# Kernel tuning notes

Measured on AMD Instinct MI355X. Metric: run time of the kernel, lower is better.

## Reference

```python
import jax, jax.numpy as jnp
import numpy as np

N, E, IN, H, C, ED = 50000, 400000, 128, 16, 32, 16
NEG_SLOPE = 0.2

def setup_inputs() -> dict:
    key = jax.random.key(0)
    ks = jax.random.split(key, 9)
    x = jax.random.normal(ks[0], (N, IN), jnp.float32)
    edge_index = jax.random.randint(ks[1], (2, E), 0, N, dtype=jnp.int32)
    edge_attr = jax.random.normal(ks[2], (E, ED), jnp.float32)
    batch = jnp.zeros((N,), jnp.int32)
    W_l = jax.random.normal(ks[3], (IN, H * C), jnp.float32) * 0.05
    W_r = jax.random.normal(ks[4], (IN, H * C), jnp.float32) * 0.05
    att = jax.random.normal(ks[5], (H, C), jnp.float32) * 0.05
    bias_gat = jax.random.normal(ks[6], (C,), jnp.float32) * 0.05
    W_res = jax.random.normal(ks[7], (IN, C), jnp.float32) * 0.05
    return {"x": x, "edge_index": edge_index, "edge_attr": edge_attr, "batch": batch,
            "W_l": W_l, "W_r": W_r, "att": att, "bias_gat": bias_gat, "W_res": W_res}

def reference(x, edge_index, edge_attr, batch, W_l, W_r, att, bias_gat, W_res):
    # GATv2Conv (heads=16, concat=False, add_self_loops=True, edge_dim=None so
    # edge_attr is unused; dropout is inference no-op), then ReLU + projected residual.
    n = x.shape[0]
    loops = jnp.arange(n, dtype=edge_index.dtype)
    src = jnp.concatenate([edge_index[0], loops])  # message source j
    dst = jnp.concatenate([edge_index[1], loops])  # message target i
    xl = (x @ W_l).reshape(n, H, C)  # source transform
    xr = (x @ W_r).reshape(n, H, C)  # target transform
    # GATv2 score: e_ij = a^T LeakyReLU(xl_j + xr_i), per head. [Etot, H]
    e = jnp.einsum('ehc,hc->eh', jax.nn.leaky_relu(xl[src] + xr[dst], NEG_SLOPE), att)
    # segment softmax over incoming edges of each destination node
    m = jax.lax.stop_gradient(jax.ops.segment_max(e, dst, num_segments=n))
    ex = jnp.exp(e - m[dst])
    s = jax.ops.segment_sum(ex, dst, num_segments=n)
    alpha = ex / (s[dst] + 1e-16)  # [Etot, H]
    # weighted scatter-aggregate of source messages
    out = jax.ops.segment_sum(xl[src] * alpha[:, :, None], dst, num_segments=n)  # [N, H, C]
    gat_out = out.mean(axis=1) + bias_gat  # concat=False -> head mean, + bias
    x_out = jax.nn.relu(gat_out) + x @ W_res  # ReLU then SkipConnection projection
    return (x_out, alpha)
```

## Files before the change

kernel.cpp:

```cpp
#include <hip/hip_runtime.h>
#include <hip/hip_bf16.h>

typedef unsigned int u32;
typedef unsigned short u16;

typedef __attribute__((ext_vector_type(8))) short bf16x8;
typedef __attribute__((ext_vector_type(4))) float f32x4;

__device__ __forceinline__ float bflo(u32 p){ union{u32 u; float f;} v; v.u = p << 16; return v.f; }
__device__ __forceinline__ float bfhi(u32 p){ union{u32 u; float f;} v; v.u = p & 0xFFFF0000u; return v.f; }
__device__ __forceinline__ u16 f2bf(float f){
    union{float f; u32 u;} v; v.f = f;
    u32 r = (v.u + 0x7FFFu + ((v.u >> 16) & 1u)) >> 16;
    return (u16)r;
}
__device__ __forceinline__ u32 pack2(float a, float b){
    return ((u32)f2bf(a)) | (((u32)f2bf(b)) << 16);
}

#define HH 16
#define CC 32
#define HC 512
#define KIN 128
#define CT 1056
#define RESCALE_THR 8.0f

__global__ __launch_bounds__(256) void k_xconv(
    const float* __restrict__ x, u16* __restrict__ xb, int total)
{
    int t = blockIdx.x * 256 + threadIdx.x;
    if (t * 8 >= total) return;
    const float4* src = (const float4*)(x + (size_t)t * 8);
    float4 a = src[0], b = src[1];
    uint4 o;
    o.x = pack2(a.x, a.y); o.y = pack2(a.z, a.w);
    o.z = pack2(b.x, b.y); o.w = pack2(b.z, b.w);
    ((uint4*)xb)[t] = o;
}

__global__ __launch_bounds__(128) void k_wconv(
    const float* __restrict__ Wl, const float* __restrict__ Wr,
    const float* __restrict__ Wres, u16* __restrict__ wbt_frag)
{
    int c = blockIdx.x;
    int t = threadIdx.x;
    int k = t;
    float v;
    if (c < 512)       v = Wl[(size_t)k * 512 + c];
    else if (c < 1024) v = Wr[(size_t)k * 512 + (c - 512)];
    else               v = Wres[(size_t)k * 32 + (c - 1024)];
    int e    = k & 7;
    int krow = k >> 3;
    int kk   = krow >> 2;
    int lane = ((krow & 3) << 4) | (c & 15);
    int ct   = c >> 4;
    wbt_frag[(((size_t)ct * 4 + kk) * 64 + lane) * 8 + e] = f2bf(v);
}

__global__ __launch_bounds__(256) void k_mfma(
    const u16* __restrict__ xb, const u16* __restrict__ wbt_frag,
    u16* __restrict__ xl, u16* __restrict__ xr, float* __restrict__ xres,
    int N, int nrb)
{
    __shared__ u16 sh[128 * 128];
    const int i = blockIdx.x;
    const int xcd = i & 7;
    const int j = i >> 3;
    const int rb = xcd + 8 * (j / 9);
    const int cb = j % 9;
    if (rb >= nrb) return;
    const int tid = threadIdx.x;
    const int wave = tid >> 6, lane = tid & 63;
    const int row0 = rb * 128;

    uint4 zero = {0, 0, 0, 0};
    #pragma unroll
    for (int it = 0; it < 8; it++) {
        int idx = tid + it * 256;
        int r = idx >> 4, ch = idx & 15;
        int grow = row0 + r;
        uint4 v = (grow < N) ? ((const uint4*)(xb + (size_t)grow * KIN))[ch] : zero;
        *(uint4*)(sh + r * 128 + ((ch ^ (r & 7)) * 8)) = v;
    }
    __syncthreads();

    bf16x8 afrag[2][4];
    #pragma unroll
    for (int mt = 0; mt < 2; mt++) {
        #pragma unroll
        for (int kk = 0; kk < 4; kk++) {
            int r = wave * 32 + mt * 16 + (lane & 15);
            int chunk = (kk * 4 + (lane >> 4)) ^ (r & 7);
            afrag[mt][kk] = *(const bf16x8*)(sh + r * 128 + chunk * 8);
        }
    }
    __syncthreads();

    if (cb < 8) {
        #pragma unroll
        for (int nt = 0; nt < 8; nt++) {
            int ct = cb * 8 + nt;
            const bf16x8* bp = (const bf16x8*)(wbt_frag + (((size_t)ct * 4) * 64 + lane) * 8);
            f32x4 acc0 = {0, 0, 0, 0}, acc1 = {0, 0, 0, 0};
            #pragma unroll
            for (int kk = 0; kk < 4; kk++) {
                bf16x8 bfrag = bp[kk * 64];
                acc0 = __builtin_amdgcn_mfma_f32_16x16x32_bf16(afrag[0][kk], bfrag, acc0, 0, 0, 0);
                acc1 = __builtin_amdgcn_mfma_f32_16x16x32_bf16(afrag[1][kk], bfrag, acc1, 0, 0, 0);
            }
            int lcol = nt * 16 + (lane & 15);
            int ch = lcol >> 3, cin = lcol & 7;
            #pragma unroll
            for (int mt = 0; mt < 2; mt++) {
                f32x4 a = (mt == 0) ? acc0 : acc1;
                int rbase = wave * 32 + mt * 16 + (lane >> 4) * 4;
                #pragma unroll
                for (int jj = 0; jj < 4; jj++) {
                    int row = rbase + jj;
                    int chs = ch ^ ((row >> 2) & 3);
                    sh[row * 128 + chs * 8 + cin] = f2bf(a[jj]);
                }
            }
        }
        __syncthreads();
        u16* out = (cb < 4) ? xl : xr;
        const int colbase = (cb & 3) * 128;
        #pragma unroll
        for (int it = 0; it < 8; it++) {
            int idx = tid + it * 256;
            int r = idx >> 4, ch = idx & 15;
            int grow = row0 + r;
            if (grow < N) {
                int chs = ch ^ ((r >> 2) & 3);
                uint4 v = *(const uint4*)(sh + r * 128 + chs * 8);
                *(uint4*)(out + (size_t)grow * HC + colbase + ch * 8) = v;
            }
        }
    } else {
        #pragma unroll
        for (int nt = 0; nt < 2; nt++) {
            int ct = 64 + nt;
            const bf16x8* bp = (const bf16x8*)(wbt_frag + (((size_t)ct * 4) * 64 + lane) * 8);
            f32x4 acc0 = {0, 0, 0, 0}, acc1 = {0, 0, 0, 0};
            #pragma unroll
            for (int kk = 0; kk < 4; kk++) {
                bf16x8 bfrag = bp[kk * 64];
                acc0 = __builtin_amdgcn_mfma_f32_16x16x32_bf16(afrag[0][kk], bfrag, acc0, 0, 0, 0);
                acc1 = __builtin_amdgcn_mfma_f32_16x16x32_bf16(afrag[1][kk], bfrag, acc1, 0, 0, 0);
            }
            int c_out = nt * 16 + (lane & 15);
            #pragma unroll
            for (int mt = 0; mt < 2; mt++) {
                f32x4 a = (mt == 0) ? acc0 : acc1;
                int rbse = row0 + wave * 32 + mt * 16 + (lane >> 4) * 4;
                #pragma unroll
                for (int jj = 0; jj < 4; jj++) {
                    int grow = rbse + jj;
                    if (grow < N) xres[(size_t)grow * CC + c_out] = a[jj];
                }
            }
        }
    }
}

__global__ __launch_bounds__(256) void k_count(
    const int* __restrict__ ei, int* __restrict__ counts, int E, int N)
{
    int e = blockIdx.x * 256 + threadIdx.x;
    if (e >= E + N) return;
    int dst = (e < E) ? ei[E + e] : e - E;
    atomicAdd(&counts[dst], 1);
}

__global__ __launch_bounds__(1024) void k_scan1(
    const int* __restrict__ counts, int* __restrict__ offs, int* __restrict__ partials, int N)
{
    __shared__ int sh[1024];
    int i = blockIdx.x * 1024 + threadIdx.x;
    int v = (i < N) ? counts[i] : 0;
    sh[threadIdx.x] = v;
    __syncthreads();
    for (int off = 1; off < 1024; off <<= 1) {
        int t = (threadIdx.x >= off) ? sh[threadIdx.x - off] : 0;
        __syncthreads();
        sh[threadIdx.x] += t;
        __syncthreads();
    }
    if (i < N) offs[i] = sh[threadIdx.x] - v;
    if (threadIdx.x == 1023) partials[blockIdx.x] = sh[1023];
}

__global__ void k_scan2(int* __restrict__ partials, int nb)
{
    if (threadIdx.x == 0 && blockIdx.x == 0) {
        int run = 0;
        for (int k = 0; k < nb; k++) { int t = partials[k]; partials[k] = run; run += t; }
    }
}

__global__ __launch_bounds__(1024) void k_scan3(
    int* __restrict__ offs, const int* __restrict__ partials, int* __restrict__ cursor, int N)
{
    int i = blockIdx.x * 1024 + threadIdx.x;
    if (i < N) {
        int o = offs[i] + partials[blockIdx.x];
        offs[i] = o;
        cursor[i] = o;
    }
}

__global__ __launch_bounds__(256) void k_scatter(
    const int* __restrict__ ei, int* __restrict__ cursor,
    int* __restrict__ src_sorted, int* __restrict__ eid_sorted, int E, int N)
{
    int e = blockIdx.x * 256 + threadIdx.x;
    if (e >= E + N) return;
    int src, dst;
    if (e < E) { src = ei[e]; dst = ei[E + e]; }
    else       { src = e - E; dst = src; }
    int pos = atomicAdd(&cursor[dst], 1);
    src_sorted[pos] = src;
    eid_sorted[pos] = e;
}

__global__ __launch_bounds__(256) void k_fused(
    const int* __restrict__ src_sorted, const int* __restrict__ eid_sorted,
    const int* __restrict__ offs, const int* __restrict__ counts,
    const u16* __restrict__ xl, const u16* __restrict__ xr, const float* __restrict__ att,
    float* __restrict__ e_out, float2* __restrict__ ms_buf,
    float* __restrict__ out_mean, int N)
{
    int wid = (blockIdx.x * 256 + threadIdx.x) >> 6;
    int lane = threadIdx.x & 63;
    if (wid >= N) return;
    const int node = wid;

    uint4 b = ((const uint4*)(xr + (size_t)node * HC))[lane];
    float xrv[8] = { bflo(b.x), bfhi(b.x), bflo(b.y), bfhi(b.y),
                     bflo(b.z), bfhi(b.z), bflo(b.w), bfhi(b.w) };
    float4 w0 = ((const float4*)att)[lane * 2];
    float4 w1 = ((const float4*)att)[lane * 2 + 1];
    float wv[8] = { w0.x, w0.y, w0.z, w0.w, w1.x, w1.y, w1.z, w1.w };

    float m = -3.402823466e38f, s = 0.f;
    float acc[8] = {0, 0, 0, 0, 0, 0, 0, 0};

    const int beg = offs[node];
    const int deg = counts[node];
    const int h = lane >> 2;

    for (int base = 0; base < deg; base += 64) {
        int cnt = min(64, deg - base);
        int my_src = 0, my_eid = 0;
        if (lane < cnt) {
            my_src = src_sorted[beg + base + lane];
            my_eid = eid_sorted[beg + base + lane];
        }
        int s0 = __shfl(my_src, 0);
        uint4 a = ((const uint4*)(xl + (size_t)s0 * HC))[lane];
        for (int t = 0; t < cnt; t++) {
            uint4 ac = a;
            {
                int sn = __shfl(my_src, min(t + 1, cnt - 1));
                a = ((const uint4*)(xl + (size_t)sn * HC))[lane];
            }
            float xv[8] = { bflo(ac.x), bfhi(ac.x), bflo(ac.y), bfhi(ac.y),
                            bflo(ac.z), bfhi(ac.z), bflo(ac.w), bfhi(ac.w) };
            float esum = 0.f;
            #pragma unroll
            for (int q = 0; q < 8; q++) {
                float v = xv[q] + xrv[q];
                v = fmaxf(v, 0.2f * v);
                esum = fmaf(v, wv[q], esum);
            }
            esum += __shfl_xor(esum, 1);
            esum += __shfl_xor(esum, 2);

            int eid = __shfl(my_eid, t);
            if ((lane & 3) == 0)
                e_out[(size_t)eid * HH + h] = esum;

            if (__any(esum > m + RESCALE_THR)) {
                float mn = fmaxf(m, esum);
                float sc = __expf(m - mn);
                float p  = __expf(esum - mn);
                s = s * sc + p;
                m = mn;
                #pragma unroll
                for (int q = 0; q < 8; q++) acc[q] = fmaf(p, xv[q], acc[q] * sc);
            } else {
                float p = __expf(esum - m);
                s += p;
                #pragma unroll
                for (int q = 0; q < 8; q++) acc[q] = fmaf(p, xv[q], acc[q]);
            }
        }
    }

    float inv = 1.f / (s + 1e-16f);
    if ((lane & 3) == 0)
        ms_buf[(size_t)node * HH + h] = make_float2(m, inv);

    #pragma unroll
    for (int q = 0; q < 8; q++) acc[q] *= inv;
    #pragma unroll
    for (int st = 4; st <= 32; st <<= 1) {
        #pragma unroll
        for (int q = 0; q < 8; q++) acc[q] += __shfl_xor(acc[q], st);
    }
    if (lane < 4) {
        float* dp = out_mean + (size_t)node * CC + lane * 8;
        #pragma unroll
        for (int q = 0; q < 8; q++) dp[q] = acc[q];
    }
}

__global__ __launch_bounds__(256) void k_alpha(
    const int* __restrict__ ei, float* __restrict__ alpha,
    const float2* __restrict__ ms_buf, int E, int N)
{
    long long i = (long long)blockIdx.x * 256 + threadIdx.x;
    long long tot = (long long)(E + N) * HH;
    if (i >= tot) return;
    int edge = (int)(i >> 4);
    int h = (int)(i & 15);
    int dst = (edge < E) ? ei[E + edge] : edge - E;
    float2 ms = ms_buf[(size_t)dst * HH + h];
    alpha[i] = __expf(alpha[i] - ms.x) * ms.y;
}

__global__ __launch_bounds__(256) void k_final(
    const float* __restrict__ out_mean, const float* __restrict__ xres,
    const float* __restrict__ bias, float* __restrict__ x_out, int N)
{
    int i = blockIdx.x * 256 + threadIdx.x;
    if (i >= N * CC) return;
    int c = i & 31;
    float g = out_mean[i] * (1.f / 16.f) + bias[c];
    g = g > 0.f ? g : 0.f;
    x_out[i] = g + xres[i];
}

extern "C" void kernel_launch(void* const* d_in, const int* in_sizes, int n_in,
                              void* d_out, int out_size, void* d_ws, size_t ws_size,
                              hipStream_t stream)
{
    const int N = in_sizes[0] / KIN;
    const int E = in_sizes[1] / 2;
    const int Etot = E + N;

    const float* x    = (const float*)d_in[0];
    const int*   ei   = (const int*)d_in[1];
    const float* Wl   = (const float*)d_in[4];
    const float* Wr   = (const float*)d_in[5];
    const float* att  = (const float*)d_in[6];
    const float* bias = (const float*)d_in[7];
    const float* Wres = (const float*)d_in[8];

    char* ws = (char*)d_ws;
    u16*   xl         = (u16*)ws;   ws += (size_t)N * HC * 2;
    u16*   xr         = (u16*)ws;   ws += (size_t)N * HC * 2;
    float2* ms_buf    = (float2*)ws; ws += (size_t)N * HH * 8;
    float* xres       = (float*)ws; ws += (size_t)N * CC * 4;
    float* out_mean   = (float*)ws; ws += (size_t)N * CC * 4;
    int*   counts     = (int*)ws;   ws += (size_t)N * 4;
    int*   offs       = (int*)ws;   ws += (size_t)N * 4;
    int*   cursor     = (int*)ws;   ws += (size_t)N * 4;
    int*   partials   = (int*)ws;   ws += 256;
    int*   src_sorted = (int*)ws;   ws += (size_t)Etot * 4;
    int*   eid_sorted = (int*)ws;   ws += (size_t)Etot * 4;
    u16*   xb         = (u16*)ws;   ws += (size_t)N * KIN * 2;
    u16*   wbt_frag   = (u16*)ws;   ws += (size_t)CT * KIN * 2;

    float* x_out     = (float*)d_out;
    float* alpha_out = x_out + (size_t)N * CC;

    hipMemsetAsync(counts, 0, (size_t)N * 4, stream);

    int xtot = N * KIN;
    k_xconv<<<(xtot / 8 + 255) / 256, 256, 0, stream>>>(x, xb, xtot);
    k_wconv<<<CT, 128, 0, stream>>>(Wl, Wr, Wres, wbt_frag);

    int nrb = (N + 127) / 128;
    int mgrid = 8 * ((nrb + 7) / 8) * 9;
    k_mfma<<<mgrid, 256, 0, stream>>>(xb, wbt_frag, xl, xr, xres, N, nrb);

    int eg = (Etot + 255) / 256;
    k_count<<<eg, 256, 0, stream>>>(ei, counts, E, N);

    int nb = (N + 1023) / 1024;
    k_scan1<<<nb, 1024, 0, stream>>>(counts, offs, partials, N);
    k_scan2<<<1, 64, 0, stream>>>(partials, nb);
    k_scan3<<<nb, 1024, 0, stream>>>(offs, partials, cursor, N);

    k_scatter<<<eg, 256, 0, stream>>>(ei, cursor, src_sorted, eid_sorted, E, N);

    k_fused<<<(N * 64 + 255) / 256, 256, 0, stream>>>(
        src_sorted, eid_sorted, offs, counts, xl, xr, att,
        alpha_out, ms_buf, out_mean, N);

    int ag = (int)(((long long)Etot * HH + 255) / 256);
    k_alpha<<<ag, 256, 0, stream>>>(ei, alpha_out, ms_buf, E, N);

    k_final<<<(N * CC + 255) / 256, 256, 0, stream>>>(out_mean, xres, bias, x_out, N);
}
```

Baseline: 213.6 us.

## Fuse prep, scan and epilogue kernels; packed f32x2 math in aggregation

Merges the x/weight conversion and the counts memset into one prep kernel. It replaces the serial scan2 plus scan3 pair with a single kernel that reduces the partials per block, and merges the alpha-normalise and final-output kernels. This removes several launches and the single-thread scan pass. The aggregation kernel now runs one 64-thread block per node, reads src and eid indices directly instead of staging them through shuffles, and uses packed 2-wide float ops meant to map to packed FP32 instructions. Per-edge scalar index loads and the smaller blocks may add load latency and scheduling overhead.

```diff
diff --git a/kernel.cpp b/kernel.cpp
--- a/kernel.cpp
+++ b/kernel.cpp
@@ -6,6 +6,7 @@
 
 typedef __attribute__((ext_vector_type(8))) short bf16x8;
 typedef __attribute__((ext_vector_type(4))) float f32x4;
+typedef __attribute__((ext_vector_type(2))) float f32x2;
 
 __device__ __forceinline__ float bflo(u32 p){ union{u32 u; float f;} v; v.u = p << 16; return v.f; }
 __device__ __forceinline__ float bfhi(u32 p){ union{u32 u; float f;} v; v.u = p & 0xFFFF0000u; return v.f; }
@@ -25,36 +26,37 @@
 #define CT 1056
 #define RESCALE_THR 8.0f
 
-__global__ __launch_bounds__(256) void k_xconv(
-    const float* __restrict__ x, u16* __restrict__ xb, int total)
+__global__ __launch_bounds__(256) void k_prep(
+    const float* __restrict__ x, const float* __restrict__ Wl,
+    const float* __restrict__ Wr, const float* __restrict__ Wres,
+    u16* __restrict__ xb, u16* __restrict__ wbt_frag, int* __restrict__ counts,
+    int xq, int N)
 {
     int t = blockIdx.x * 256 + threadIdx.x;
-    if (t * 8 >= total) return;
-    const float4* src = (const float4*)(x + (size_t)t * 8);
-    float4 a = src[0], b = src[1];
-    uint4 o;
-    o.x = pack2(a.x, a.y); o.y = pack2(a.z, a.w);
-    o.z = pack2(b.x, b.y); o.w = pack2(b.z, b.w);
-    ((uint4*)xb)[t] = o;
-}
-
-__global__ __launch_bounds__(128) void k_wconv(
-    const float* __restrict__ Wl, const float* __restrict__ Wr,
-    const float* __restrict__ Wres, u16* __restrict__ wbt_frag)
-{
-    int c = blockIdx.x;
-    int t = threadIdx.x;
-    int k = t;
-    float v;
-    if (c < 512)       v = Wl[(size_t)k * 512 + c];
-    else if (c < 1024) v = Wr[(size_t)k * 512 + (c - 512)];
-    else               v = Wres[(size_t)k * 32 + (c - 1024)];
-    int e    = k & 7;
-    int krow = k >> 3;
-    int kk   = krow >> 2;
-    int lane = ((krow & 3) << 4) | (c & 15);
-    int ct   = c >> 4;
-    wbt_frag[(((size_t)ct * 4 + kk) * 64 + lane) * 8 + e] = f2bf(v);
+    if (t < xq) {
+        const float4* src = (const float4*)(x + (size_t)t * 8);
+        float4 a = src[0], b = src[1];
+        uint4 o;
+        o.x = pack2(a.x, a.y); o.y = pack2(a.z, a.w);
+        o.z = pack2(b.x, b.y); o.w = pack2(b.z, b.w);
+        ((uint4*)xb)[t] = o;
+    } else if (t < xq + CT * 128) {
+        int u = t - xq;
+        int c = u >> 7;
+        int k = u & 127;
+        float v;
+        if (c < 512)       v = Wl[(size_t)k * 512 + c];
+        else if (c < 1024) v = Wr[(size_t)k * 512 + (c - 512)];
+        else               v = Wres[(size_t)k * 32 + (c - 1024)];
+        int e    = k & 7;
+        int krow = k >> 3;
+        int kk   = krow >> 2;
+        int lane = ((krow & 3) << 4) | (c & 15);
+        int ct   = c >> 4;
+        wbt_frag[(((size_t)ct * 4 + kk) * 64 + lane) * 8 + e] = f2bf(v);
+    } else if (t < xq + CT * 128 + N) {
+        counts[t - xq - CT * 128] = 0;
+    }
 }
 
 __global__ __launch_bounds__(256) void k_mfma(
@@ -190,20 +192,22 @@
     if (threadIdx.x == 1023) partials[blockIdx.x] = sh[1023];
 }
 
-__global__ void k_scan2(int* __restrict__ partials, int nb)
-{
-    if (threadIdx.x == 0 && blockIdx.x == 0) {
-        int run = 0;
-        for (int k = 0; k < nb; k++) { int t = partials[k]; partials[k] = run; run += t; }
-    }
-}
-
-__global__ __launch_bounds__(1024) void k_scan3(
-    int* __restrict__ offs, const int* __restrict__ partials, int* __restrict__ cursor, int N)
-{
+__global__ __launch_bounds__(1024) void k_scan3f(
+    int* __restrict__ offs, const int* __restrict__ partials,
+    int* __restrict__ cursor, int N, int nb)
+{
+    __shared__ int sbase;
+    if (threadIdx.x < 64) {
+        int k = threadIdx.x;
+        int v = (k < nb && k < blockIdx.x) ? partials[k] : 0;
+        #pragma unroll
+        for (int st = 1; st < 64; st <<= 1) v += __shfl_xor(v, st);
+        if (threadIdx.x == 0) sbase = v;
+    }
+    __syncthreads();
     int i = blockIdx.x * 1024 + threadIdx.x;
     if (i < N) {
-        int o = offs[i] + partials[blockIdx.x];
+        int o = offs[i] + sbase;
         offs[i] = o;
         cursor[i] = o;
     }
@@ -223,77 +227,76 @@
     eid_sorted[pos] = e;
 }
 
-__global__ __launch_bounds__(256) void k_fused(
+__global__ __launch_bounds__(64) void k_fused(
     const int* __restrict__ src_sorted, const int* __restrict__ eid_sorted,
     const int* __restrict__ offs, const int* __restrict__ counts,
     const u16* __restrict__ xl, const u16* __restrict__ xr, const float* __restrict__ att,
     float* __restrict__ e_out, float2* __restrict__ ms_buf,
     float* __restrict__ out_mean, int N)
 {
-    int wid = (blockIdx.x * 256 + threadIdx.x) >> 6;
-    int lane = threadIdx.x & 63;
-    if (wid >= N) return;
-    const int node = wid;
+    const int node = blockIdx.x;
+    const int lane = threadIdx.x;
+    const int h = lane >> 2;
 
     uint4 b = ((const uint4*)(xr + (size_t)node * HC))[lane];
-    float xrv[8] = { bflo(b.x), bfhi(b.x), bflo(b.y), bfhi(b.y),
-                     bflo(b.z), bfhi(b.z), bflo(b.w), bfhi(b.w) };
+    f32x2 xr0 = {bflo(b.x), bfhi(b.x)}, xr1 = {bflo(b.y), bfhi(b.y)};
+    f32x2 xr2 = {bflo(b.z), bfhi(b.z)}, xr3 = {bflo(b.w), bfhi(b.w)};
     float4 w0 = ((const float4*)att)[lane * 2];
     float4 w1 = ((const float4*)att)[lane * 2 + 1];
-    float wv[8] = { w0.x, w0.y, w0.z, w0.w, w1.x, w1.y, w1.z, w1.w };
+    f32x2 wv0 = {w0.x, w0.y}, wv1 = {w0.z, w0.w};
+    f32x2 wv2 = {w1.x, w1.y}, wv3 = {w1.z, w1.w};
 
     float m = -3.402823466e38f, s = 0.f;
-    float acc[8] = {0, 0, 0, 0, 0, 0, 0, 0};
+    f32x2 ac0 = {0,0}, ac1 = {0,0}, ac2 = {0,0}, ac3 = {0,0};
 
     const int beg = offs[node];
     const int deg = counts[node];
-    const int h = lane >> 2;
-
-    for (int base = 0; base < deg; base += 64) {
-        int cnt = min(64, deg - base);
-        int my_src = 0, my_eid = 0;
-        if (lane < cnt) {
-            my_src = src_sorted[beg + base + lane];
-            my_eid = eid_sorted[beg + base + lane];
-        }
-        int s0 = __shfl(my_src, 0);
-        uint4 a = ((const uint4*)(xl + (size_t)s0 * HC))[lane];
-        for (int t = 0; t < cnt; t++) {
-            uint4 ac = a;
-            {
-                int sn = __shfl(my_src, min(t + 1, cnt - 1));
-                a = ((const uint4*)(xl + (size_t)sn * HC))[lane];
-            }
-            float xv[8] = { bflo(ac.x), bfhi(ac.x), bflo(ac.y), bfhi(ac.y),
-                            bflo(ac.z), bfhi(ac.z), bflo(ac.w), bfhi(ac.w) };
-            float esum = 0.f;
-            #pragma unroll
-            for (int q = 0; q < 8; q++) {
-                float v = xv[q] + xrv[q];
-                v = fmaxf(v, 0.2f * v);
-                esum = fmaf(v, wv[q], esum);
-            }
-            esum += __shfl_xor(esum, 1);
-            esum += __shfl_xor(esum, 2);
-
-            int eid = __shfl(my_eid, t);
-            if ((lane & 3) == 0)
-                e_out[(size_t)eid * HH + h] = esum;
-
-            if (__any(esum > m + RESCALE_THR)) {
-                float mn = fmaxf(m, esum);
-                float sc = __expf(m - mn);
-                float p  = __expf(esum - mn);
-                s = s * sc + p;
-                m = mn;
-                #pragma unroll
-                for (int q = 0; q < 8; q++) acc[q] = fmaf(p, xv[q], acc[q] * sc);
-            } else {
-                float p = __expf(esum - m);
-                s += p;
-                #pragma unroll
-                for (int q = 0; q < 8; q++) acc[q] = fmaf(p, xv[q], acc[q]);
-            }
+
+    int sv = src_sorted[beg];
+    uint4 a = ((const uint4*)(xl + (size_t)sv * HC))[lane];
+    for (int t = 0; t < deg; t++) {
+        uint4 acr = a;
+        int sn = src_sorted[beg + min(t + 1, deg - 1)];
+        a = ((const uint4*)(xl + (size_t)sn * HC))[lane];
+
+        f32x2 xv0 = {bflo(acr.x), bfhi(acr.x)};
+        f32x2 xv1 = {bflo(acr.y), bfhi(acr.y)};
+        f32x2 xv2 = {bflo(acr.z), bfhi(acr.z)};
+        f32x2 xv3 = {bflo(acr.w), bfhi(acr.w)};
+
+        f32x2 es2 = {0.f, 0.f};
+        f32x2 v;
+        v = xv0 + xr0; v = __builtin_elementwise_max(v, 0.2f * v); es2 = __builtin_elementwise_fma(v, wv0, es2);
+        v = xv1 + xr1; v = __builtin_elementwise_max(v, 0.2f * v); es2 = __builtin_elementwise_fma(v, wv1, es2);
+        v = xv2 + xr2; v = __builtin_elementwise_max(v, 0.2f * v); es2 = __builtin_elementwise_fma(v, wv2, es2);
+        v = xv3 + xr3; v = __builtin_elementwise_max(v, 0.2f * v); es2 = __builtin_elementwise_fma(v, wv3, es2);
+        float esum = es2.x + es2.y;
+        esum += __shfl_xor(esum, 1);
+        esum += __shfl_xor(esum, 2);
+
+        int eid = eid_sorted[beg + t];
+        if ((lane & 3) == 0)
+            e_out[(size_t)eid * HH + h] = esum;
+
+        if (__any(esum > m + RESCALE_THR)) {
+            float mn = fmaxf(m, esum);
+            float sc = __expf(m - mn);
+            float p  = __expf(esum - mn);
+            s = s * sc + p;
+            m = mn;
+            f32x2 p2 = {p, p}, sc2 = {sc, sc};
+            ac0 = __builtin_elementwise_fma(p2, xv0, ac0 * sc2);
+            ac1 = __builtin_elementwise_fma(p2, xv1, ac1 * sc2);
+            ac2 = __builtin_elementwise_fma(p2, xv2, ac2 * sc2);
+            ac3 = __builtin_elementwise_fma(p2, xv3, ac3 * sc2);
+        } else {
+            float p = __expf(esum - m);
+            s += p;
+            f32x2 p2 = {p, p};
+            ac0 = __builtin_elementwise_fma(p2, xv0, ac0);
+            ac1 = __builtin_elementwise_fma(p2, xv1, ac1);
+            ac2 = __builtin_elementwise_fma(p2, xv2, ac2);
+            ac3 = __builtin_elementwise_fma(p2, xv3, ac3);
         }
     }
 
@@ -301,8 +304,8 @@
     if ((lane & 3) == 0)
         ms_buf[(size_t)node * HH + h] = make_float2(m, inv);
 
-    #pragma unroll
-    for (int q = 0; q < 8; q++) acc[q] *= inv;
+    float acc[8] = { ac0.x * inv, ac0.y * inv, ac1.x * inv, ac1.y * inv,
+                     ac2.x * inv, ac2.y * inv, ac3.x * inv, ac3.y * inv };
     #pragma unroll
     for (int st = 4; st <= 32; st <<= 1) {
         #pragma unroll
@@ -315,30 +318,27 @@
     }
 }
 
-__global__ __launch_bounds__(256) void k_alpha(
+__global__ __launch_bounds__(256) void k_alphafinal(
     const int* __restrict__ ei, float* __restrict__ alpha,
-    const float2* __restrict__ ms_buf, int E, int N)
+    const float2* __restrict__ ms_buf, const float* __restrict__ out_mean,
+    const float* __restrict__ xres, const float* __restrict__ bias,
+    float* __restrict__ x_out, int E, int N)
 {
     long long i = (long long)blockIdx.x * 256 + threadIdx.x;
+    if (i < (long long)N * CC) {
+        int c = (int)(i & 31);
+        float g = out_mean[i] * (1.f / 16.f) + bias[c];
+        g = g > 0.f ? g : 0.f;
+        x_out[i] = g + xres[i];
+    }
     long long tot = (long long)(E + N) * HH;
-    if (i >= tot) return;
-    int edge = (int)(i >> 4);
-    int h = (int)(i & 15);
-    int dst = (edge < E) ? ei[E + edge] : edge - E;
-    float2 ms = ms_buf[(size_t)dst * HH + h];
-    alpha[i] = __expf(alpha[i] - ms.x) * ms.y;
-}
-
-__global__ __launch_bounds__(256) void k_final(
-    const float* __restrict__ out_mean, const float* __restrict__ xres,
-    const float* __restrict__ bias, float* __restrict__ x_out, int N)
-{
-    int i = blockIdx.x * 256 + threadIdx.x;
-    if (i >= N * CC) return;
-    int c = i & 31;
-    float g = out_mean[i] * (1.f / 16.f) + bias[c];
-    g = g > 0.f ? g : 0.f;
-    x_out[i] = g + xres[i];
+    if (i < tot) {
+        int edge = (int)(i >> 4);
+        int h = (int)(i & 15);
+        int dst = (edge < E) ? ei[E + edge] : edge - E;
+        float2 ms = ms_buf[(size_t)dst * HH + h];
+        alpha[i] = __expf(alpha[i] - ms.x) * ms.y;
+    }
 }
 
 extern "C" void kernel_launch(void* const* d_in, const int* in_sizes, int n_in,
@@ -375,11 +375,10 @@
     float* x_out     = (float*)d_out;
     float* alpha_out = x_out + (size_t)N * CC;
 
-    hipMemsetAsync(counts, 0, (size_t)N * 4, stream);
-
-    int xtot = N * KIN;
-    k_xconv<<<(xtot / 8 + 255) / 256, 256, 0, stream>>>(x, xb, xtot);
-    k_wconv<<<CT, 128, 0, stream>>>(Wl, Wr, Wres, wbt_frag);
+    int xq = N * KIN / 8;
+    int ptot = xq + CT * 128 + N;
+    k_prep<<<(ptot + 255) / 256, 256, 0, stream>>>(
+        x, Wl, Wr, Wres, xb, wbt_frag, counts, xq, N);
 
     int nrb = (N + 127) / 128;
     int mgrid = 8 * ((nrb + 7) / 8) * 9;
@@ -387,20 +386,16 @@
 
     int eg = (Etot + 255) / 256;
     k_count<<<eg, 256, 0, stream>>>(ei, counts, E, N);
-
     int nb = (N + 1023) / 1024;
     k_scan1<<<nb, 1024, 0, stream>>>(counts, offs, partials, N);
-    k_scan2<<<1, 64, 0, stream>>>(partials, nb);
-    k_scan3<<<nb, 1024, 0, stream>>>(offs, partials, cursor, N);
-
+    k_scan3f<<<nb, 1024, 0, stream>>>(offs, partials, cursor, N, nb);
     k_scatter<<<eg, 256, 0, stream>>>(ei, cursor, src_sorted, eid_sorted, E, N);
 
-    k_fused<<<(N * 64 + 255) / 256, 256, 0, stream>>>(
+    k_fused<<<N, 64, 0, stream>>>(
         src_sorted, eid_sorted, offs, counts, xl, xr, att,
         alpha_out, ms_buf, out_mean, N);
 
-    int ag = (int)(((long long)Etot * HH + 255) / 256);
-    k_alpha<<<ag, 256, 0, stream>>>(ei, alpha_out, ms_buf, E, N);
-
-    k_final<<<(N * CC + 255) / 256, 256, 0, stream>>>(out_mean, xres, bias, x_out, N);
-}
+    long long tot = (long long)Etot * HH;
+    k_alphafinal<<<(int)((tot + 255) / 256), 256, 0, stream>>>(
+        ei, alpha_out, ms_buf, out_mean, xres, bias, x_out, E, N);
+}
```

After: 190.0 us. 11.1% less time.
